# Performance work log

Hardware: AMD Instinct MI355X
Metric: run time of the kernel (lower is better)

## Reference

```python
import jax, jax.numpy as jnp
import numpy as np

D_IN = 1024
D_OUT = 1024
NUM_HEADS = 16
HEAD_DIM = D_OUT // NUM_HEADS


def setup_inputs() -> dict:
    key = jax.random.key(0)
    k_x, k_q, k_k, k_v, k_o = jax.random.split(key, 5)
    # Xavier-uniform-ish init for weights (stored as [d_in, d_out] for x @ W)
    lim = float(np.sqrt(6.0 / (D_IN + D_OUT)) / np.sqrt(2.0))
    lim_o = float(np.sqrt(6.0 / (D_OUT + D_OUT)))
    return {
        "x": jax.random.normal(k_x, (2, 2048, D_IN), dtype=jnp.float32),
        "W_query": jax.random.uniform(k_q, (D_IN, D_OUT), jnp.float32, -lim, lim),
        "W_key": jax.random.uniform(k_k, (D_IN, D_OUT), jnp.float32, -lim, lim),
        "W_value": jax.random.uniform(k_v, (D_IN, D_OUT), jnp.float32, -lim, lim),
        "W_out": jax.random.uniform(k_o, (D_OUT, D_OUT), jnp.float32, -lim_o, lim_o),
        "b_out": jnp.zeros((D_OUT,), dtype=jnp.float32),
    }


def reference(x, W_query, W_key, W_value, W_out, b_out):
    B, S, _ = x.shape
    scale = 1.0 / np.sqrt(HEAD_DIM)

    def split_heads(t):  # [B,S,D] -> [B,H,S,hd]
        return t.reshape(B, S, NUM_HEADS, HEAD_DIM).transpose(0, 2, 1, 3)

    q = split_heads(x @ W_query)
    k = split_heads(x @ W_key)
    v = split_heads(x @ W_value)

    scores = jnp.einsum("bhqd,bhkd->bhqk", q, k) * scale  # [B,H,S,S]
    causal = jnp.tril(jnp.ones((S, S), dtype=bool))  # True = keep
    scores = jnp.where(causal, scores, -jnp.inf)
    weights = jax.nn.softmax(scores, axis=-1)
    ctx = jnp.einsum("bhqk,bhkd->bhqd", weights, v)
    ctx = ctx.transpose(0, 2, 1, 3).reshape(B, S, D_OUT)
    return ctx @ W_out + b_out
```

## Files before the change

kernel.cpp:

```cpp
#include <hip/hip_runtime.h>
#include <hip/hip_bf16.h>


typedef __bf16 bf16_t;
typedef __bf16 bf16x4 __attribute__((ext_vector_type(4)));
typedef __bf16 bf16x8 __attribute__((ext_vector_type(8)));
typedef float f32x4 __attribute__((ext_vector_type(4)));

__device__ __forceinline__ void barrier_lgkm() {
    asm volatile("s_waitcnt lgkmcnt(0)\n\ts_barrier" ::: "memory");
}

__device__ __forceinline__ float exp_pwrite(f32x4 sc[4], bf16_t* Ps,
                                            int quad, int l16) {
    float part = 0.f;
    int rowbase = l16 * 64;
    int gran = (quad & 1) * 4;
    int chi = quad >> 1;
#pragma unroll
    for (int nt = 0; nt < 4; nt++) {
        f32x4 p;
#pragma unroll
        for (int rr = 0; rr < 4; rr++) {
            p[rr] = __builtin_amdgcn_exp2f(sc[nt][rr]);
            part += p[rr];
        }
        bf16x4 pb;
#pragma unroll
        for (int rr = 0; rr < 4; rr++) pb[rr] = (bf16_t)p[rr];
        int cc = (nt * 2 + chi) ^ (l16 & 7);
        *(bf16x4*)(Ps + rowbase + cc * 8 + gran) = pb;
    }
    part += __shfl_xor(part, 16);
    part += __shfl_xor(part, 32);
    return part;
}

__global__ __launch_bounds__(256) void prep_k(
    const float* __restrict__ x, const float* __restrict__ W0,
    const float* __restrict__ W1, const float* __restrict__ W2,
    const float* __restrict__ W3, bf16_t* __restrict__ xb,
    bf16_t* __restrict__ WTs) {
    __shared__ bf16_t T[64][65];
    int t = threadIdx.x;
    int blk = blockIdx.x;
    if (blk < 4096) {
        int i = blk * 256 + t;
        float4 v = ((const float4*)x)[i];
        bf16x4 o;
        o[0] = (bf16_t)v.x; o[1] = (bf16_t)v.y;
        o[2] = (bf16_t)v.z; o[3] = (bf16_t)v.w;
        ((bf16x4*)xb)[i] = o;
        return;
    }
    int jj = blk - 4096;
    int k0 = (jj & 15) * 64, n0 = ((jj >> 4) & 15) * 64, z = jj >> 8;
    const float* W = (z == 0) ? W0 : (z == 1) ? W1 : (z == 2) ? W2 : W3;
    bf16_t* WT = WTs + (size_t)z * 1048576;
#pragma unroll
    for (int c = 0; c < 4; c++) {
        int idx = c * 256 + t;
        int row = idx >> 4, col4 = (idx & 15) * 4;
        float4 v = *(const float4*)(W + (k0 + row) * 1024 + n0 + col4);
        T[row][col4 + 0] = (bf16_t)v.x;
        T[row][col4 + 1] = (bf16_t)v.y;
        T[row][col4 + 2] = (bf16_t)v.z;
        T[row][col4 + 3] = (bf16_t)v.w;
    }
    __syncthreads();
#pragma unroll
    for (int c = 0; c < 4; c++) {
        int idx = c * 256 + t;
        int nrow = idx >> 4, kc4 = (idx & 15) * 4;
        bf16x4 o;
        o[0] = T[kc4 + 0][nrow];
        o[1] = T[kc4 + 1][nrow];
        o[2] = T[kc4 + 2][nrow];
        o[3] = T[kc4 + 3][nrow];
        *(bf16x4*)(WT + (n0 + nrow) * 1024 + k0 + kc4) = o;
    }
}

__global__ __launch_bounds__(256) void qkv_k(
    const bf16_t* __restrict__ xb, const bf16_t* __restrict__ WTs,
    bf16_t* __restrict__ Qb, bf16_t* __restrict__ Kb, bf16_t* __restrict__ Vb) {
    const int KD = 1024;
    __shared__ __align__(16) bf16_t As[2][4096];
    __shared__ __align__(16) bf16_t Bs[2][4096];
    int tid = threadIdx.x;
    int wave = tid >> 6, lane = tid & 63;
    int quad = lane >> 4, l16 = lane & 15;
    int wm = wave >> 1, wn = wave & 1;
    int z = blockIdx.z;
    const bf16_t* BT = WTs + (size_t)z * 1048576;
    int m0 = blockIdx.x * 128;
    int n0 = blockIdx.y * 128;

    int r = tid >> 2;
    int c8 = (((tid & 3) ^ ((tid >> 3) & 3))) * 8;
    const bf16_t* gA0 = xb + (size_t)(m0 + r) * KD + c8;
    const bf16_t* gA1 = xb + (size_t)(m0 + 64 + r) * KD + c8;
    const bf16_t* gB0 = BT + (size_t)(n0 + r) * KD + c8;
    const bf16_t* gB1 = BT + (size_t)(n0 + 64 + r) * KD + c8;

    f32x4 acc[4][4];
#pragma unroll
    for (int i = 0; i < 4; i++)
#pragma unroll
        for (int j = 0; j < 4; j++) acc[i][j] = (f32x4){0.f, 0.f, 0.f, 0.f};

    int4 sa0 = *(const int4*)gA0, sa1 = *(const int4*)gA1;
    int4 sb0 = *(const int4*)gB0, sb1 = *(const int4*)gB1;
    *(int4*)(As[0] + tid * 8) = sa0;
    *(int4*)(As[0] + 2048 + tid * 8) = sa1;
    *(int4*)(Bs[0] + tid * 8) = sb0;
    *(int4*)(Bs[0] + 2048 + tid * 8) = sb1;
    sa0 = *(const int4*)(gA0 + 32); sa1 = *(const int4*)(gA1 + 32);
    sb0 = *(const int4*)(gB0 + 32); sb1 = *(const int4*)(gB1 + 32);

    int csw = (quad ^ ((l16 >> 1) & 3)) * 8;
#pragma unroll 1
    for (int kk = 0; kk < 32; kk += 2) {
        barrier_lgkm();
        bf16x8 af[4], bfr[4];
#pragma unroll
        for (int mt = 0; mt < 4; mt++)
            af[mt] = *(const bf16x8*)(As[0] + (wm * 64 + mt * 16 + l16) * 32 + csw);
#pragma unroll
        for (int nt = 0; nt < 4; nt++)
            bfr[nt] = *(const bf16x8*)(Bs[0] + (wn * 64 + nt * 16 + l16) * 32 + csw);
        *(int4*)(As[1] + tid * 8) = sa0;
        *(int4*)(As[1] + 2048 + tid * 8) = sa1;
        *(int4*)(Bs[1] + tid * 8) = sb0;
        *(int4*)(Bs[1] + 2048 + tid * 8) = sb1;
        if (kk + 2 < 32) {
            int k0 = (kk + 2) * 32;
            sa0 = *(const int4*)(gA0 + k0); sa1 = *(const int4*)(gA1 + k0);
            sb0 = *(const int4*)(gB0 + k0); sb1 = *(const int4*)(gB1 + k0);
        }
        if (z == 2) {
#pragma unroll
            for (int mt = 0; mt < 4; mt++)
#pragma unroll
                for (int nt = 0; nt < 4; nt++)
                    acc[mt][nt] = __builtin_amdgcn_mfma_f32_16x16x32_bf16(
                        bfr[nt], af[mt], acc[mt][nt], 0, 0, 0);
        } else {
#pragma unroll
            for (int mt = 0; mt < 4; mt++)
#pragma unroll
                for (int nt = 0; nt < 4; nt++)
                    acc[mt][nt] = __builtin_amdgcn_mfma_f32_16x16x32_bf16(
                        af[mt], bfr[nt], acc[mt][nt], 0, 0, 0);
        }
        barrier_lgkm();
#pragma unroll
        for (int mt = 0; mt < 4; mt++)
            af[mt] = *(const bf16x8*)(As[1] + (wm * 64 + mt * 16 + l16) * 32 + csw);
#pragma unroll
        for (int nt = 0; nt < 4; nt++)
            bfr[nt] = *(const bf16x8*)(Bs[1] + (wn * 64 + nt * 16 + l16) * 32 + csw);
        if (kk + 2 < 32) {
            *(int4*)(As[0] + tid * 8) = sa0;
            *(int4*)(As[0] + 2048 + tid * 8) = sa1;
            *(int4*)(Bs[0] + tid * 8) = sb0;
            *(int4*)(Bs[0] + 2048 + tid * 8) = sb1;
            if (kk + 3 < 32) {
                int k0 = (kk + 3) * 32;
                sa0 = *(const int4*)(gA0 + k0); sa1 = *(const int4*)(gA1 + k0);
                sb0 = *(const int4*)(gB0 + k0); sb1 = *(const int4*)(gB1 + k0);
            }
        }
        if (z == 2) {
#pragma unroll
            for (int mt = 0; mt < 4; mt++)
#pragma unroll
                for (int nt = 0; nt < 4; nt++)
                    acc[mt][nt] = __builtin_amdgcn_mfma_f32_16x16x32_bf16(
                        bfr[nt], af[mt], acc[mt][nt], 0, 0, 0);
        } else {
#pragma unroll
            for (int mt = 0; mt < 4; mt++)
#pragma unroll
                for (int nt = 0; nt < 4; nt++)
                    acc[mt][nt] = __builtin_amdgcn_mfma_f32_16x16x32_bf16(
                        af[mt], bfr[nt], acc[mt][nt], 0, 0, 0);
        }
    }

    if (z == 0) {
#pragma unroll
        for (int mt = 0; mt < 4; mt++) {
            int mg_base = m0 + wm * 64 + mt * 16 + quad * 4;
#pragma unroll
            for (int nt = 0; nt < 4; nt++) {
                int ng = n0 + wn * 64 + nt * 16 + l16;
                int h = ng >> 6, d = ng & 63;
#pragma unroll
                for (int rr = 0; rr < 4; rr++) {
                    int mg = mg_base + rr;
                    int b = mg >> 11, s = mg & 2047;
                    Qb[(((size_t)(b * 16 + h) * 2048) + s) * 64 + d] =
                        (bf16_t)acc[mt][nt][rr];
                }
            }
        }
    } else if (z == 1) {
#pragma unroll
        for (int mt = 0; mt < 4; mt++) {
            int mg_base = m0 + wm * 64 + mt * 16 + quad * 4;
#pragma unroll
            for (int nt = 0; nt < 4; nt++) {
                int ng = n0 + wn * 64 + nt * 16 + l16;
                int h = ng >> 6, dd = ng & 63;
#pragma unroll
                for (int rr = 0; rr < 4; rr++) {
                    int mg = mg_base + rr;
                    int b = mg >> 11, sl = mg & 2047;
                    int kt = sl >> 6, row = sl & 63;
                    int cc = (dd >> 3) ^ (row & 7);
                    Kb[(size_t)(b * 16 + h) * 131072 + kt * 4096 + row * 64 +
                       cc * 8 + (dd & 7)] = (bf16_t)acc[mt][nt][rr];
                }
            }
        }
    } else {
#pragma unroll
        for (int mt = 0; mt < 4; mt++) {
            int sg = m0 + wm * 64 + mt * 16 + l16;
            int b = sg >> 11, sl = sg & 2047;
            int kt = sl >> 6, srow = sl & 63;
#pragma unroll
            for (int nt = 0; nt < 4; nt++) {
                int dg_base = n0 + wn * 64 + nt * 16 + quad * 4;
#pragma unroll
                for (int rr = 0; rr < 4; rr++) {
                    int dg = dg_base + rr;
                    int h = dg >> 6, dd = dg & 63;
                    int cc = (srow >> 3) ^ (dd & 7);
                    Vb[(size_t)(b * 16 + h) * 131072 + kt * 4096 + dd * 64 +
                       cc * 8 + (srow & 7)] = (bf16_t)acc[mt][nt][rr];
                }
            }
        }
    }
}

__global__ __launch_bounds__(64) void attn_k(
    const bf16_t* __restrict__ Qb, const bf16_t* __restrict__ Kb,
    const bf16_t* __restrict__ Vb, bf16_t* __restrict__ ctxb) {
    const int S = 2048;
    __shared__ __align__(16) bf16_t Ps[2][1024];
    int lane = threadIdx.x & 63;
    int quad = lane >> 4, l16 = lane & 15;

    int f = blockIdx.x;
    int xcd = f & 7;
    int r = f >> 3;
    int qtj = 15 - (r >> 4);
    int rl = r & 15;
    int bh = xcd * 4 + (rl >> 2);
    int wgrp = rl & 3;
    int h = bh & 15, b = bh >> 4;
    int q0 = qtj * 128;

    const bf16_t* Qbh = Qb + (size_t)bh * S * 64;
    const bf16_t* Kbh = Kb + (size_t)bh * 131072;
    const bf16_t* Vbh = Vb + (size_t)bh * 131072;

    const float qs = 0.125f * 1.44269504f;
    bf16x8 aQ[2][2];
#pragma unroll
    for (int sub = 0; sub < 2; sub++) {
        const bf16_t* rq = Qbh + (size_t)(q0 + sub * 64 + wgrp * 16 + l16) * 64;
#pragma unroll
        for (int ks = 0; ks < 2; ks++) {
            bf16x8 t = *(const bf16x8*)(rq + ks * 32 + quad * 8);
#pragma unroll
            for (int jj = 0; jj < 8; jj++) t[jj] = (bf16_t)((float)t[jj] * qs);
            aQ[sub][ks] = t;
        }
    }

    float L[2] = {0.f, 0.f};
    f32x4 O[2][4];
#pragma unroll
    for (int sub = 0; sub < 2; sub++)
#pragma unroll
        for (int i = 0; i < 4; i++) O[sub][i] = (f32x4){0.f, 0.f, 0.f, 0.f};

    int koff[4][2];
#pragma unroll
    for (int nt = 0; nt < 4; nt++)
#pragma unroll
        for (int ks = 0; ks < 2; ks++)
            koff[nt][ks] = (nt * 16 + l16) * 64 + ((ks * 4 + quad) ^ (l16 & 7)) * 8;

    int tmax = 2 * qtj + 2;
#pragma unroll 1
    for (int kt = 0; kt < tmax; kt++) {
        const bf16_t* kbase = Kbh + kt * 4096;
        const bf16_t* vbase = Vbh + kt * 4096;
        bf16x8 kf[4][2], vf[4][2];
#pragma unroll
        for (int nt = 0; nt < 4; nt++)
#pragma unroll
            for (int ks = 0; ks < 2; ks++) {
                kf[nt][ks] = *(const bf16x8*)(kbase + koff[nt][ks]);
                vf[nt][ks] = *(const bf16x8*)(vbase + koff[nt][ks]);
            }

        bool do_lo = (kt < tmax - 1);
        if (do_lo) {
            f32x4 sc[4];
#pragma unroll
            for (int nt = 0; nt < 4; nt++) {
                f32x4 ss = (f32x4){0.f, 0.f, 0.f, 0.f};
                ss = __builtin_amdgcn_mfma_f32_16x16x32_bf16(kf[nt][0], aQ[0][0], ss, 0, 0, 0);
                ss = __builtin_amdgcn_mfma_f32_16x16x32_bf16(kf[nt][1], aQ[0][1], ss, 0, 0, 0);
                sc[nt] = ss;
            }
            if (kt == tmax - 2) {
                int qg = q0 + wgrp * 16 + l16;
#pragma unroll
                for (int nt = 0; nt < 4; nt++)
#pragma unroll
                    for (int rr = 0; rr < 4; rr++)
                        if (kt * 64 + nt * 16 + quad * 4 + rr > qg) sc[nt][rr] = -1e30f;
            }
            L[0] += exp_pwrite(sc, Ps[0], quad, l16);
        }
        {
            f32x4 sc[4];
#pragma unroll
            for (int nt = 0; nt < 4; nt++) {
                f32x4 ss = (f32x4){0.f, 0.f, 0.f, 0.f};
                ss = __builtin_amdgcn_mfma_f32_16x16x32_bf16(kf[nt][0], aQ[1][0], ss, 0, 0, 0);
                ss = __builtin_amdgcn_mfma_f32_16x16x32_bf16(kf[nt][1], aQ[1][1], ss, 0, 0, 0);
                sc[nt] = ss;
            }
            if (kt == tmax - 1) {
                int qg = q0 + 64 + wgrp * 16 + l16;
#pragma unroll
                for (int nt = 0; nt < 4; nt++)
#pragma unroll
                    for (int rr = 0; rr < 4; rr++)
                        if (kt * 64 + nt * 16 + quad * 4 + rr > qg) sc[nt][rr] = -1e30f;
            }
            L[1] += exp_pwrite(sc, Ps[1], quad, l16);
        }

#pragma unroll
        for (int ks = 0; ks < 2; ks++) {
            int csw = ((ks * 4 + quad) ^ (l16 & 7)) * 8;
            bf16x8 aPhi = *(const bf16x8*)(Ps[1] + l16 * 64 + csw);
            bf16x8 aPlo;
            if (do_lo) aPlo = *(const bf16x8*)(Ps[0] + l16 * 64 + csw);
#pragma unroll
            for (int nt = 0; nt < 4; nt++) {
                O[1][nt] = __builtin_amdgcn_mfma_f32_16x16x32_bf16(aPhi, vf[nt][ks],
                                                                   O[1][nt], 0, 0, 0);
                if (do_lo)
                    O[0][nt] = __builtin_amdgcn_mfma_f32_16x16x32_bf16(aPlo, vf[nt][ks],
                                                                       O[0][nt], 0, 0, 0);
            }
        }
    }

#pragma unroll
    for (int sub = 0; sub < 2; sub++) {
        float il[4];
#pragma unroll
        for (int rr = 0; rr < 4; rr++) il[rr] = 1.f / __shfl(L[sub], quad * 4 + rr);
#pragma unroll
        for (int nt = 0; nt < 4; nt++) {
#pragma unroll
            for (int rr = 0; rr < 4; rr++) {
                int qoff = q0 + sub * 64 + wgrp * 16 + quad * 4 + rr;
                int col = h * 64 + nt * 16 + l16;
                ctxb[(size_t)(b * 2048 + qoff) * 1024 + col] =
                    (bf16_t)(O[sub][nt][rr] * il[rr]);
            }
        }
    }
}

__global__ __launch_bounds__(256) void out_k(
    const bf16_t* __restrict__ ctxb, const bf16_t* __restrict__ WoT,
    const float* __restrict__ bo, float* __restrict__ out) {
    const int KD = 1024;
    __shared__ __align__(16) bf16_t As[2][2048];
    __shared__ __align__(16) bf16_t Bs[2][4096];
    int tid = threadIdx.x;
    int wave = tid >> 6, lane = tid & 63;
    int quad = lane >> 4, l16 = lane & 15;
    int wm = wave >> 1, wn = wave & 1;
    int m0 = blockIdx.x * 64;
    int n0 = blockIdx.y * 128;

    int r = tid >> 2;
    int c8 = (((tid & 3) ^ ((tid >> 3) & 3))) * 8;
    const bf16_t* gA  = ctxb + (size_t)(m0 + r) * KD + c8;
    const bf16_t* gB0 = WoT + (size_t)(n0 + r) * KD + c8;
    const bf16_t* gB1 = WoT + (size_t)(n0 + 64 + r) * KD + c8;

    f32x4 acc[2][4];
#pragma unroll
    for (int i = 0; i < 2; i++)
#pragma unroll
        for (int j = 0; j < 4; j++) acc[i][j] = (f32x4){0.f, 0.f, 0.f, 0.f};

    int4 sa = *(const int4*)gA;
    int4 sb0 = *(const int4*)gB0, sb1 = *(const int4*)gB1;
    *(int4*)(As[0] + tid * 8) = sa;
    *(int4*)(Bs[0] + tid * 8) = sb0;
    *(int4*)(Bs[0] + 2048 + tid * 8) = sb1;
    sa = *(const int4*)(gA + 32);
    sb0 = *(const int4*)(gB0 + 32); sb1 = *(const int4*)(gB1 + 32);

    int csw = (quad ^ ((l16 >> 1) & 3)) * 8;
#pragma unroll 1
    for (int kk = 0; kk < 32; kk += 2) {
        barrier_lgkm();
        bf16x8 af[2], bfr[4];
#pragma unroll
        for (int mt = 0; mt < 2; mt++)
            af[mt] = *(const bf16x8*)(As[0] + (wm * 32 + mt * 16 + l16) * 32 + csw);
#pragma unroll
        for (int nt = 0; nt < 4; nt++)
            bfr[nt] = *(const bf16x8*)(Bs[0] + (wn * 64 + nt * 16 + l16) * 32 + csw);
        *(int4*)(As[1] + tid * 8) = sa;
        *(int4*)(Bs[1] + tid * 8) = sb0;
        *(int4*)(Bs[1] + 2048 + tid * 8) = sb1;
        if (kk + 2 < 32) {
            int k0 = (kk + 2) * 32;
            sa = *(const int4*)(gA + k0);
            sb0 = *(const int4*)(gB0 + k0); sb1 = *(const int4*)(gB1 + k0);
        }
#pragma unroll
        for (int mt = 0; mt < 2; mt++)
#pragma unroll
            for (int nt = 0; nt < 4; nt++)
                acc[mt][nt] = __builtin_amdgcn_mfma_f32_16x16x32_bf16(
                    af[mt], bfr[nt], acc[mt][nt], 0, 0, 0);
        barrier_lgkm();
#pragma unroll
        for (int mt = 0; mt < 2; mt++)
            af[mt] = *(const bf16x8*)(As[1] + (wm * 32 + mt * 16 + l16) * 32 + csw);
#pragma unroll
        for (int nt = 0; nt < 4; nt++)
            bfr[nt] = *(const bf16x8*)(Bs[1] + (wn * 64 + nt * 16 + l16) * 32 + csw);
        if (kk + 2 < 32) {
            *(int4*)(As[0] + tid * 8) = sa;
            *(int4*)(Bs[0] + tid * 8) = sb0;
            *(int4*)(Bs[0] + 2048 + tid * 8) = sb1;
            if (kk + 3 < 32) {
                int k0 = (kk + 3) * 32;
                sa = *(const int4*)(gA + k0);
                sb0 = *(const int4*)(gB0 + k0); sb1 = *(const int4*)(gB1 + k0);
            }
        }
#pragma unroll
        for (int mt = 0; mt < 2; mt++)
#pragma unroll
            for (int nt = 0; nt < 4; nt++)
                acc[mt][nt] = __builtin_amdgcn_mfma_f32_16x16x32_bf16(
                    af[mt], bfr[nt], acc[mt][nt], 0, 0, 0);
    }

#pragma unroll
    for (int mt = 0; mt < 2; mt++) {
        int mg_base = m0 + wm * 32 + mt * 16 + quad * 4;
#pragma unroll
        for (int nt = 0; nt < 4; nt++) {
            int ng = n0 + wn * 64 + nt * 16 + l16;
            float bv = bo[ng];
#pragma unroll
            for (int rr = 0; rr < 4; rr++) {
                int mg = mg_base + rr;
                out[(size_t)mg * 1024 + ng] = acc[mt][nt][rr] + bv;
            }
        }
    }
}

extern "C" void kernel_launch(void* const* d_in, const int* in_sizes, int n_in,
                              void* d_out, int out_size, void* d_ws, size_t ws_size,
                              hipStream_t stream) {
    const float* x  = (const float*)d_in[0];
    const float* Wq = (const float*)d_in[1];
    const float* Wk = (const float*)d_in[2];
    const float* Wv = (const float*)d_in[3];
    const float* Wo = (const float*)d_in[4];
    const float* bo = (const float*)d_in[5];
    float* out = (float*)d_out;
    char* ws = (char*)d_ws;

    bf16_t* xb   = (bf16_t*)ws;
    bf16_t* WTs  = (bf16_t*)(ws + (8u << 20));
    bf16_t* Qb   = (bf16_t*)(ws + (16u << 20));
    bf16_t* Kb   = (bf16_t*)(ws + (24u << 20));
    bf16_t* Vb   = (bf16_t*)(ws + (32u << 20));
    bf16_t* ctxb = (bf16_t*)(ws + (40u << 20));

    prep_k<<<5120, 256, 0, stream>>>(x, Wq, Wk, Wv, Wo, xb, WTs);
    qkv_k<<<dim3(32, 8, 3), 256, 0, stream>>>(xb, WTs, Qb, Kb, Vb);
    attn_k<<<2048, 64, 0, stream>>>(Qb, Kb, Vb, ctxb);
    out_k<<<dim3(64, 8), 256, 0, stream>>>(ctxb, WTs + 3145728, bo, out);
}
```

Before: 176.0 us.

## Pre-tile GEMM operands into fragment-major layout and load MFMA fragments directly from global

The prep kernel now writes x and the transposed weights in a 16x32 blocked, fragment-major layout, so each MFMA operand fragment is one contiguous 16-byte global load. The QKV and output projection GEMMs drop their LDS double-buffering and barriers and read fragments straight from global memory (through L2/L1), with a simple unrolled k-loop. This removes LDS traffic and synchronisation. In exchange it loses explicit software prefetch and the cross-wave data sharing LDS gave, so latency hiding and redundant global reads now rely on the caches and on occupancy.

```diff
diff --git a/kernel.cpp b/kernel.cpp
--- a/kernel.cpp
+++ b/kernel.cpp
@@ -6,35 +6,6 @@
 typedef __bf16 bf16x4 __attribute__((ext_vector_type(4)));
 typedef __bf16 bf16x8 __attribute__((ext_vector_type(8)));
 typedef float f32x4 __attribute__((ext_vector_type(4)));
-
-__device__ __forceinline__ void barrier_lgkm() {
-    asm volatile("s_waitcnt lgkmcnt(0)\n\ts_barrier" ::: "memory");
-}
-
-__device__ __forceinline__ float exp_pwrite(f32x4 sc[4], bf16_t* Ps,
-                                            int quad, int l16) {
-    float part = 0.f;
-    int rowbase = l16 * 64;
-    int gran = (quad & 1) * 4;
-    int chi = quad >> 1;
-#pragma unroll
-    for (int nt = 0; nt < 4; nt++) {
-        f32x4 p;
-#pragma unroll
-        for (int rr = 0; rr < 4; rr++) {
-            p[rr] = __builtin_amdgcn_exp2f(sc[nt][rr]);
-            part += p[rr];
-        }
-        bf16x4 pb;
-#pragma unroll
-        for (int rr = 0; rr < 4; rr++) pb[rr] = (bf16_t)p[rr];
-        int cc = (nt * 2 + chi) ^ (l16 & 7);
-        *(bf16x4*)(Ps + rowbase + cc * 8 + gran) = pb;
-    }
-    part += __shfl_xor(part, 16);
-    part += __shfl_xor(part, 32);
-    return part;
-}
 
 __global__ __launch_bounds__(256) void prep_k(
     const float* __restrict__ x, const float* __restrict__ W0,
@@ -46,11 +17,15 @@
     int blk = blockIdx.x;
     if (blk < 4096) {
         int i = blk * 256 + t;
+        int row = i >> 8;
+        int k4 = (i & 255) * 4;
         float4 v = ((const float4*)x)[i];
         bf16x4 o;
         o[0] = (bf16_t)v.x; o[1] = (bf16_t)v.y;
         o[2] = (bf16_t)v.z; o[3] = (bf16_t)v.w;
-        ((bf16x4*)xb)[i] = o;
+        size_t dst = ((size_t)((row >> 4) * 32 + (k4 >> 5))) * 512 +
+                     (row & 15) * 32 + (k4 & 31);
+        *(bf16x4*)(xb + dst) = o;
         return;
     }
     int jj = blk - 4096;
@@ -77,16 +52,16 @@
         o[1] = T[kc4 + 1][nrow];
         o[2] = T[kc4 + 2][nrow];
         o[3] = T[kc4 + 3][nrow];
-        *(bf16x4*)(WT + (n0 + nrow) * 1024 + k0 + kc4) = o;
+        int n = n0 + nrow, k = k0 + kc4;
+        size_t dst = ((size_t)((n >> 4) * 32 + (k >> 5))) * 512 +
+                     (n & 15) * 32 + (k & 31);
+        *(bf16x4*)(WT + dst) = o;
     }
 }
 
 __global__ __launch_bounds__(256) void qkv_k(
-    const bf16_t* __restrict__ xb, const bf16_t* __restrict__ WTs,
+    const bf16_t* __restrict__ xA, const bf16_t* __restrict__ WTs,
     bf16_t* __restrict__ Qb, bf16_t* __restrict__ Kb, bf16_t* __restrict__ Vb) {
-    const int KD = 1024;
-    __shared__ __align__(16) bf16_t As[2][4096];
-    __shared__ __align__(16) bf16_t Bs[2][4096];
     int tid = threadIdx.x;
     int wave = tid >> 6, lane = tid & 63;
     int quad = lane >> 4, l16 = lane & 15;
@@ -95,13 +70,9 @@
     const bf16_t* BT = WTs + (size_t)z * 1048576;
     int m0 = blockIdx.x * 128;
     int n0 = blockIdx.y * 128;
-
-    int r = tid >> 2;
-    int c8 = (((tid & 3) ^ ((tid >> 3) & 3))) * 8;
-    const bf16_t* gA0 = xb + (size_t)(m0 + r) * KD + c8;
-    const bf16_t* gA1 = xb + (size_t)(m0 + 64 + r) * KD + c8;
-    const bf16_t* gB0 = BT + (size_t)(n0 + r) * KD + c8;
-    const bf16_t* gB1 = BT + (size_t)(n0 + 64 + r) * KD + c8;
+    int mblk = (m0 >> 4) + wm * 4;
+    int nblk = (n0 >> 4) + wn * 4;
+    int lofs = l16 * 32 + quad * 8;
 
     f32x4 acc[4][4];
 #pragma unroll
@@ -109,68 +80,15 @@
 #pragma unroll
         for (int j = 0; j < 4; j++) acc[i][j] = (f32x4){0.f, 0.f, 0.f, 0.f};
 
-    int4 sa0 = *(const int4*)gA0, sa1 = *(const int4*)gA1;
-    int4 sb0 = *(const int4*)gB0, sb1 = *(const int4*)gB1;
-    *(int4*)(As[0] + tid * 8) = sa0;
-    *(int4*)(As[0] + 2048 + tid * 8) = sa1;
-    *(int4*)(Bs[0] + tid * 8) = sb0;
-    *(int4*)(Bs[0] + 2048 + tid * 8) = sb1;
-    sa0 = *(const int4*)(gA0 + 32); sa1 = *(const int4*)(gA1 + 32);
-    sb0 = *(const int4*)(gB0 + 32); sb1 = *(const int4*)(gB1 + 32);
-
-    int csw = (quad ^ ((l16 >> 1) & 3)) * 8;
-#pragma unroll 1
-    for (int kk = 0; kk < 32; kk += 2) {
-        barrier_lgkm();
+#pragma unroll 2
+    for (int kk = 0; kk < 32; kk++) {
         bf16x8 af[4], bfr[4];
 #pragma unroll
         for (int mt = 0; mt < 4; mt++)
-            af[mt] = *(const bf16x8*)(As[0] + (wm * 64 + mt * 16 + l16) * 32 + csw);
+            af[mt] = *(const bf16x8*)(xA + ((size_t)((mblk + mt) * 32 + kk)) * 512 + lofs);
 #pragma unroll
         for (int nt = 0; nt < 4; nt++)
-            bfr[nt] = *(const bf16x8*)(Bs[0] + (wn * 64 + nt * 16 + l16) * 32 + csw);
-        *(int4*)(As[1] + tid * 8) = sa0;
-        *(int4*)(As[1] + 2048 + tid * 8) = sa1;
-        *(int4*)(Bs[1] + tid * 8) = sb0;
-        *(int4*)(Bs[1] + 2048 + tid * 8) = sb1;
-        if (kk + 2 < 32) {
-            int k0 = (kk + 2) * 32;
-            sa0 = *(const int4*)(gA0 + k0); sa1 = *(const int4*)(gA1 + k0);
-            sb0 = *(const int4*)(gB0 + k0); sb1 = *(const int4*)(gB1 + k0);
-        }
-        if (z == 2) {
-#pragma unroll
-            for (int mt = 0; mt < 4; mt++)
-#pragma unroll
-                for (int nt = 0; nt < 4; nt++)
-                    acc[mt][nt] = __builtin_amdgcn_mfma_f32_16x16x32_bf16(
-                        bfr[nt], af[mt], acc[mt][nt], 0, 0, 0);
-        } else {
-#pragma unroll
-            for (int mt = 0; mt < 4; mt++)
-#pragma unroll
-                for (int nt = 0; nt < 4; nt++)
-                    acc[mt][nt] = __builtin_amdgcn_mfma_f32_16x16x32_bf16(
-                        af[mt], bfr[nt], acc[mt][nt], 0, 0, 0);
-        }
-        barrier_lgkm();
-#pragma unroll
-        for (int mt = 0; mt < 4; mt++)
-            af[mt] = *(const bf16x8*)(As[1] + (wm * 64 + mt * 16 + l16) * 32 + csw);
-#pragma unroll
-        for (int nt = 0; nt < 4; nt++)
-            bfr[nt] = *(const bf16x8*)(Bs[1] + (wn * 64 + nt * 16 + l16) * 32 + csw);
-        if (kk + 2 < 32) {
-            *(int4*)(As[0] + tid * 8) = sa0;
-            *(int4*)(As[0] + 2048 + tid * 8) = sa1;
-            *(int4*)(Bs[0] + tid * 8) = sb0;
-            *(int4*)(Bs[0] + 2048 + tid * 8) = sb1;
-            if (kk + 3 < 32) {
-                int k0 = (kk + 3) * 32;
-                sa0 = *(const int4*)(gA0 + k0); sa1 = *(const int4*)(gA1 + k0);
-                sb0 = *(const int4*)(gB0 + k0); sb1 = *(const int4*)(gB1 + k0);
-            }
-        }
+            bfr[nt] = *(const bf16x8*)(BT + ((size_t)((nblk + nt) * 32 + kk)) * 512 + lofs);
         if (z == 2) {
 #pragma unroll
             for (int mt = 0; mt < 4; mt++)
@@ -244,6 +162,31 @@
             }
         }
     }
+}
+
+__device__ __forceinline__ float exp_pwrite(f32x4 sc[4], bf16_t* Ps,
+                                            int quad, int l16) {
+    float part = 0.f;
+    int rowbase = l16 * 64;
+    int gran = (quad & 1) * 4;
+    int chi = quad >> 1;
+#pragma unroll
+    for (int nt = 0; nt < 4; nt++) {
+        f32x4 p;
+#pragma unroll
+        for (int rr = 0; rr < 4; rr++) {
+            p[rr] = __builtin_amdgcn_exp2f(sc[nt][rr]);
+            part += p[rr];
+        }
+        bf16x4 pb;
+#pragma unroll
+        for (int rr = 0; rr < 4; rr++) pb[rr] = (bf16_t)p[rr];
+        int cc = (nt * 2 + chi) ^ (l16 & 7);
+        *(bf16x4*)(Ps + rowbase + cc * 8 + gran) = pb;
+    }
+    part += __shfl_xor(part, 16);
+    part += __shfl_xor(part, 32);
+    return part;
 }
 
 __global__ __launch_bounds__(64) void attn_k(
@@ -388,21 +331,14 @@
 __global__ __launch_bounds__(256) void out_k(
     const bf16_t* __restrict__ ctxb, const bf16_t* __restrict__ WoT,
     const float* __restrict__ bo, float* __restrict__ out) {
-    const int KD = 1024;
-    __shared__ __align__(16) bf16_t As[2][2048];
-    __shared__ __align__(16) bf16_t Bs[2][4096];
     int tid = threadIdx.x;
     int wave = tid >> 6, lane = tid & 63;
     int quad = lane >> 4, l16 = lane & 15;
     int wm = wave >> 1, wn = wave & 1;
     int m0 = blockIdx.x * 64;
     int n0 = blockIdx.y * 128;
-
-    int r = tid >> 2;
-    int c8 = (((tid & 3) ^ ((tid >> 3) & 3))) * 8;
-    const bf16_t* gA  = ctxb + (size_t)(m0 + r) * KD + c8;
-    const bf16_t* gB0 = WoT + (size_t)(n0 + r) * KD + c8;
-    const bf16_t* gB1 = WoT + (size_t)(n0 + 64 + r) * KD + c8;
+    int nblk = (n0 >> 4) + wn * 4;
+    int lofs = l16 * 32 + quad * 8;
 
     f32x4 acc[2][4];
 #pragma unroll
@@ -410,56 +346,16 @@
 #pragma unroll
         for (int j = 0; j < 4; j++) acc[i][j] = (f32x4){0.f, 0.f, 0.f, 0.f};
 
-    int4 sa = *(const int4*)gA;
-    int4 sb0 = *(const int4*)gB0, sb1 = *(const int4*)gB1;
-    *(int4*)(As[0] + tid * 8) = sa;
-    *(int4*)(Bs[0] + tid * 8) = sb0;
-    *(int4*)(Bs[0] + 2048 + tid * 8) = sb1;
-    sa = *(const int4*)(gA + 32);
-    sb0 = *(const int4*)(gB0 + 32); sb1 = *(const int4*)(gB1 + 32);
-
-    int csw = (quad ^ ((l16 >> 1) & 3)) * 8;
-#pragma unroll 1
-    for (int kk = 0; kk < 32; kk += 2) {
-        barrier_lgkm();
+#pragma unroll 2
+    for (int kk = 0; kk < 32; kk++) {
         bf16x8 af[2], bfr[4];
 #pragma unroll
         for (int mt = 0; mt < 2; mt++)
-            af[mt] = *(const bf16x8*)(As[0] + (wm * 32 + mt * 16 + l16) * 32 + csw);
+            af[mt] = *(const bf16x8*)(ctxb +
+                (size_t)(m0 + wm * 32 + mt * 16 + l16) * 1024 + kk * 32 + quad * 8);
 #pragma unroll
         for (int nt = 0; nt < 4; nt++)
-            bfr[nt] = *(const bf16x8*)(Bs[0] + (wn * 64 + nt * 16 + l16) * 32 + csw);
-        *(int4*)(As[1] + tid * 8) = sa;
-        *(int4*)(Bs[1] + tid * 8) = sb0;
-        *(int4*)(Bs[1] + 2048 + tid * 8) = sb1;
-        if (kk + 2 < 32) {
-            int k0 = (kk + 2) * 32;
-            sa = *(const int4*)(gA + k0);
-            sb0 = *(const int4*)(gB0 + k0); sb1 = *(const int4*)(gB1 + k0);
-        }
-#pragma unroll
-        for (int mt = 0; mt < 2; mt++)
-#pragma unroll
-            for (int nt = 0; nt < 4; nt++)
-                acc[mt][nt] = __builtin_amdgcn_mfma_f32_16x16x32_bf16(
-                    af[mt], bfr[nt], acc[mt][nt], 0, 0, 0);
-        barrier_lgkm();
-#pragma unroll
-        for (int mt = 0; mt < 2; mt++)
-            af[mt] = *(const bf16x8*)(As[1] + (wm * 32 + mt * 16 + l16) * 32 + csw);
-#pragma unroll
-        for (int nt = 0; nt < 4; nt++)
-            bfr[nt] = *(const bf16x8*)(Bs[1] + (wn * 64 + nt * 16 + l16) * 32 + csw);
-        if (kk + 2 < 32) {
-            *(int4*)(As[0] + tid * 8) = sa;
-            *(int4*)(Bs[0] + tid * 8) = sb0;
-            *(int4*)(Bs[0] + 2048 + tid * 8) = sb1;
-            if (kk + 3 < 32) {
-                int k0 = (kk + 3) * 32;
-                sa = *(const int4*)(gA + k0);
-                sb0 = *(const int4*)(gB0 + k0); sb1 = *(const int4*)(gB1 + k0);
-            }
-        }
+            bfr[nt] = *(const bf16x8*)(WoT + ((size_t)((nblk + nt) * 32 + kk)) * 512 + lofs);
 #pragma unroll
         for (int mt = 0; mt < 2; mt++)
 #pragma unroll
```

Result: slower. 206.4 us (+17.3%).
